# Performance work log

Hardware: AMD Instinct MI355X
Metric: run time of the kernel (lower is better)

The kernel has to match this reference:

```python
import jax, jax.numpy as jnp
import numpy as np

NUM_HEADS = 12
HEAD_DIM = 64
LOGIT_SCALE_MAX = 4.605170185988092  # log(1/0.01), open_clip default
EPS = 1e-12  # F.normalize eps


def setup_inputs() -> dict:
    key = jax.random.key(0)
    ks = jax.random.split(key, 8)
    N, L, C = 2, 2048, 768
    return {
        "x": jax.random.normal(ks[0], (N, L, C), dtype=jnp.float32),
        "in_proj_w": jax.random.normal(ks[1], (3 * C, C), dtype=jnp.float32) * 0.02,
        "in_proj_b": jax.random.normal(ks[2], (3 * C,), dtype=jnp.float32) * 0.02,
        "logit_scale": jax.random.normal(ks[3], (NUM_HEADS, 1, 1), dtype=jnp.float32),
        "learned_scale": jnp.ones((NUM_HEADS,), dtype=jnp.float32),
        "out_proj_w": jax.random.normal(ks[4], (C, C), dtype=jnp.float32) * 0.02,
        "out_proj_b": jax.random.normal(ks[5], (C,), dtype=jnp.float32) * 0.02,
        "attn_mask": jnp.zeros((L, L), dtype=jnp.float32),
    }


def _l2norm(t):
    # F.normalize(dim=-1): x / max(||x||, eps)
    n = jnp.linalg.norm(t, axis=-1, keepdims=True)
    return t / jnp.maximum(n, EPS)


def reference(x, in_proj_w, in_proj_b, logit_scale, learned_scale,
              out_proj_w, out_proj_b, attn_mask):
    N, L, C = x.shape
    H, D = NUM_HEADS, HEAD_DIM
    # packed QKV projection: [N, L, 3C]
    qkv = jnp.einsum("nlc,fc->nlf", x, in_proj_w) + in_proj_b
    q, k, v = jnp.split(qkv, 3, axis=-1)
    # [N, L, C] -> [N, H, L, D]
    to_heads = lambda t: t.reshape(N, L, H, D).transpose(0, 2, 1, 3)
    q, k, v = to_heads(q), to_heads(k), to_heads(v)
    # cosine attention with clamped exp logit scale per head
    attn = jnp.einsum("nhld,nhmd->nhlm", _l2norm(q), _l2norm(k))
    ls = jnp.exp(jnp.minimum(logit_scale, LOGIT_SCALE_MAX))  # [H,1,1]
    attn = attn * ls[None]  # broadcast over [N,H,L,L]
    attn = attn + attn_mask  # additive mask [L,L]
    attn = jax.nn.softmax(attn, axis=-1)
    out = jnp.einsum("nhlm,nhmd->nhld", attn, v)
    # learned per-head output scale
    out = out * learned_scale[None, :, None, None]
    # [N,H,L,D] -> [N,L,C]
    out = out.transpose(0, 2, 1, 3).reshape(N, L, C)
    out = jnp.einsum("nlc,fc->nlf", out, out_proj_w) + out_proj_b
    return out
```

## Files before the change

### kernel.cpp

```cpp
#include <hip/hip_runtime.h>
#include <math.h>

#define NB   2
#define SEQ  2048
#define CH   768
#define NH   12
#define HD   64
#define F3   2304
#define LSMAX 4.605170185988092f
#define LOG2E 1.4426950408889634f

typedef _Float16 f16;
typedef __attribute__((ext_vector_type(8))) _Float16 f16x8;
typedef __attribute__((ext_vector_type(4))) _Float16 f16x4;
typedef __attribute__((ext_vector_type(2))) _Float16 f16x2;
typedef __attribute__((ext_vector_type(4))) float f32x4;
typedef __attribute__((ext_vector_type(16))) float f32x16;

typedef __attribute__((address_space(3))) void lds_void;
typedef __attribute__((address_space(1))) const void gbl_cvoid;

#define QSZ   3145728
#define OATT  (3 * QSZ)
#define XHOFF 12582912
#define W1OFF 15728640
#define W2OFF 17498112
#define FLAGO 18087936

#define VCH   2048
#define VPLN  131072

#define GP2  72

__global__ __launch_bounds__(256) void cvt_f16(const float* __restrict__ X,
                                               const float* __restrict__ W1,
                                               const float* __restrict__ W2,
                                               const float* __restrict__ M,
                                               f16* __restrict__ Xh,
                                               f16* __restrict__ W1h,
                                               f16* __restrict__ W2h,
                                               int* __restrict__ flag)
{
    int tid = blockIdx.x * 256 + threadIdx.x;
    if (blockIdx.y == 3) {
        if (tid < 1048576) {
            float4 v = ((const float4*)M)[tid];
            bool nz = (v.x != 0.f) || (v.y != 0.f) || (v.z != 0.f) || (v.w != 0.f);
            if (__any(nz) && (threadIdx.x & 63) == 0) atomicOr(flag, 1);
        }
        return;
    }
    const float* src; f16* dst; int n4;
    switch (blockIdx.y) {
        case 0:  src = X;  dst = Xh;  n4 = 786432;  break;
        case 1:  src = W1; dst = W1h; n4 = 442368;  break;
        default: src = W2; dst = W2h; n4 = 147456;  break;
    }
    if (tid < n4) {
        float4 v = ((const float4*)src)[tid];
        f16x4 o = {(f16)v.x, (f16)v.y, (f16)v.z, (f16)v.w};
        ((f16x4*)dst)[tid] = o;
    }
}

__global__ __launch_bounds__(256, 4) void qkv_gemm(const f16* __restrict__ Xh,
                                                   const f16* __restrict__ Wh,
                                                   const float* __restrict__ bias,
                                                   const float* __restrict__ logit_scale,
                                                   f16* __restrict__ qkv16)
{
    __shared__ f16 As[2][128 * 32];
    __shared__ f16 Bs[2][128 * 32];
    const int t    = threadIdx.x;
    const int w    = t >> 6;
    const int lane = t & 63;
    const int quad = lane >> 4;
    const int sub  = lane & 15;
    const int wm   = w & 1, wn = w >> 1;
    const int f0   = blockIdx.x * 128;
    const int m0   = blockIdx.y * 128;

    const int s0 = t, s1 = 256 + t;
    const int r0 = s0 >> 2, cb0 = ((s0 & 3) ^ (r0 & 3)) * 8;
    const int r1 = s1 >> 2, cb1 = ((s1 & 3) ^ (r1 & 3)) * 8;
    const f16* ga0 = Xh + (size_t)(m0 + r0) * CH + cb0;
    const f16* ga1 = Xh + (size_t)(m0 + r1) * CH + cb1;
    const f16* gb0 = Wh + (size_t)(f0 + r0) * CH + cb0;
    const f16* gb1 = Wh + (size_t)(f0 + r1) * CH + cb1;

    f32x4 acc[4][4];
#pragma unroll
    for (int i = 0; i < 4; ++i)
#pragma unroll
        for (int j = 0; j < 4; ++j) acc[i][j] = (f32x4){0.f, 0.f, 0.f, 0.f};

    const int pch = (quad ^ (sub & 3)) * 8;

    __builtin_amdgcn_global_load_lds((gbl_cvoid*)(ga0), (lds_void*)&As[0][s0 * 8], 16, 0, 0);
    __builtin_amdgcn_global_load_lds((gbl_cvoid*)(ga1), (lds_void*)&As[0][s1 * 8], 16, 0, 0);
    __builtin_amdgcn_global_load_lds((gbl_cvoid*)(gb0), (lds_void*)&Bs[0][s0 * 8], 16, 0, 0);
    __builtin_amdgcn_global_load_lds((gbl_cvoid*)(gb1), (lds_void*)&Bs[0][s1 * 8], 16, 0, 0);
    __syncthreads();

    for (int k0 = 0; k0 < CH; k0 += 32) {
        const int cur = (k0 >> 5) & 1, nxt = cur ^ 1;
        if (k0 + 32 < CH) {
            __builtin_amdgcn_global_load_lds((gbl_cvoid*)(ga0 + k0 + 32), (lds_void*)&As[nxt][s0 * 8], 16, 0, 0);
            __builtin_amdgcn_global_load_lds((gbl_cvoid*)(ga1 + k0 + 32), (lds_void*)&As[nxt][s1 * 8], 16, 0, 0);
            __builtin_amdgcn_global_load_lds((gbl_cvoid*)(gb0 + k0 + 32), (lds_void*)&Bs[nxt][s0 * 8], 16, 0, 0);
            __builtin_amdgcn_global_load_lds((gbl_cvoid*)(gb1 + k0 + 32), (lds_void*)&Bs[nxt][s1 * 8], 16, 0, 0);
        }
        f16x8 af[4], bf[4];
#pragma unroll
        for (int i = 0; i < 4; ++i) {
            af[i] = *(const f16x8*)&As[cur][(wm * 64 + i * 16 + sub) * 32 + pch];
            bf[i] = *(const f16x8*)&Bs[cur][(wn * 64 + i * 16 + sub) * 32 + pch];
        }
#pragma unroll
        for (int i = 0; i < 4; ++i)
#pragma unroll
            for (int j = 0; j < 4; ++j)
                acc[i][j] = __builtin_amdgcn_mfma_f32_16x16x32_f16(af[i], bf[j], acc[i][j], 0, 0, 0);
        __syncthreads();
    }

    const int t3 = f0 / CH;
    const int h  = ((f0 + wn * 64) % CH) >> 6;
    float bb[4];
#pragma unroll
    for (int j = 0; j < 4; ++j) bb[j] = bias[f0 + wn * 64 + j * 16 + sub];

    if (t3 == 2) {
        f16* vdst = qkv16 + (size_t)2 * QSZ;
#pragma unroll
        for (int i = 0; i < 4; ++i) {
            int mb = m0 + wm * 64 + i * 16 + quad * 4;
            int nn = mb >> 11, l0 = mb & 2047;
            f16* pl = vdst + (size_t)(nn * NH + h) * VPLN + (l0 >> 5) * VCH + (l0 & 31);
#pragma unroll
            for (int j = 0; j < 4; ++j) {
                f16x4 vv;
#pragma unroll
                for (int r = 0; r < 4; ++r) vv[r] = (f16)(acc[i][j][r] + bb[j]);
                *(f16x4*)(pl + (j * 16 + sub) * 32) = vv;
            }
        }
        return;
    }

    f16* dst = qkv16 + (size_t)t3 * QSZ;
    float lsv = (t3 == 0) ? __expf(fminf(logit_scale[h], LSMAX)) * LOG2E : 1.0f;
#pragma unroll
    for (int i = 0; i < 4; ++i) {
#pragma unroll
        for (int r = 0; r < 4; ++r) {
            int m = m0 + wm * 64 + i * 16 + quad * 4 + r;
            int n = m >> 11, l = m & 2047;
            float v[4];
#pragma unroll
            for (int j = 0; j < 4; ++j) v[j] = acc[i][j][r] + bb[j];
            float ss = v[0] * v[0] + v[1] * v[1] + v[2] * v[2] + v[3] * v[3];
#pragma unroll
            for (int mk = 1; mk < 16; mk <<= 1) ss += __shfl_xor(ss, mk, 64);
            float scale = 1.0f / fmaxf(sqrtf(ss), 1e-12f);
            if (t3 == 0) scale *= lsv;
            f16* drow = dst + (((size_t)n * NH + h) * SEQ + l) * HD;
#pragma unroll
            for (int j = 0; j < 4; ++j)
                drow[j * 16 + sub] = (f16)(v[j] * scale);
        }
    }
}

union V8 { f16x4 h[2]; f16x8 v; };
union U8 { int i[4]; f16x8 v; };

__device__ __forceinline__ void compute_chunk(
    const f16x8& k0f, const f16x8& k1f, const f16x8& k2f, const f16x8& k3f,
    const V8& u0v, const V8& u1v, const V8& u2v, const V8& u3v,
    const f16x8& qf0, const f16x8& qf1, const f16x8& qf2, const f16x8& qf3,
    int cc, bool has_mask, const float* __restrict__ Mg, int h2,
    f32x16& o0, f32x16& o1, float& m_run, float& l_acc)
{
    const f16x2 one2 = {(f16)1.f, (f16)1.f};
    f32x16 sA = {};
    sA = __builtin_amdgcn_mfma_f32_32x32x16_f16(k0f, qf0, sA, 0, 0, 0);
    sA = __builtin_amdgcn_mfma_f32_32x32x16_f16(k1f, qf1, sA, 0, 0, 0);
    sA = __builtin_amdgcn_mfma_f32_32x32x16_f16(k2f, qf2, sA, 0, 0, 0);
    sA = __builtin_amdgcn_mfma_f32_32x32x16_f16(k3f, qf3, sA, 0, 0, 0);
    if (has_mask) {
#pragma unroll
        for (int rr = 0; rr < 16; ++rr) {
            int kk = cc * 32 + (rr & 3) + 8 * (rr >> 2) + 4 * h2;
            sA[rr] += LOG2E * Mg[kk];
        }
    }
    float mloc = sA[0];
#pragma unroll
    for (int rr = 1; rr < 16; ++rr) mloc = fmaxf(mloc, sA[rr]);
    float mfull = fmaxf(mloc, __shfl_xor(mloc, 32, 64));
    float mnew = fmaxf(m_run, mfull);
    float al = exp2f(m_run - mnew);
    m_run = mnew;
    l_acc *= al;
#pragma unroll
    for (int rr = 0; rr < 16; ++rr) { o0[rr] *= al; o1[rr] *= al; }
#pragma unroll
    for (int rr = 0; rr < 16; ++rr) sA[rr] = exp2f(sA[rr] - m_run);
#define PK(a, b) ({ f16x2 _t = {(f16)(a), (f16)(b)}; __builtin_bit_cast(int, _t); })
    U8 u0, u1;
    u0.i[0] = PK(sA[0], sA[1]);   u0.i[1] = PK(sA[2], sA[3]);
    u0.i[2] = PK(sA[4], sA[5]);   u0.i[3] = PK(sA[6], sA[7]);
    u1.i[0] = PK(sA[8], sA[9]);   u1.i[1] = PK(sA[10], sA[11]);
    u1.i[2] = PK(sA[12], sA[13]); u1.i[3] = PK(sA[14], sA[15]);
#undef PK
    l_acc = __builtin_amdgcn_fdot2(__builtin_bit_cast(f16x2, u0.i[0]), one2, l_acc, false);
    l_acc = __builtin_amdgcn_fdot2(__builtin_bit_cast(f16x2, u0.i[1]), one2, l_acc, false);
    l_acc = __builtin_amdgcn_fdot2(__builtin_bit_cast(f16x2, u0.i[2]), one2, l_acc, false);
    l_acc = __builtin_amdgcn_fdot2(__builtin_bit_cast(f16x2, u0.i[3]), one2, l_acc, false);
    l_acc = __builtin_amdgcn_fdot2(__builtin_bit_cast(f16x2, u1.i[0]), one2, l_acc, false);
    l_acc = __builtin_amdgcn_fdot2(__builtin_bit_cast(f16x2, u1.i[1]), one2, l_acc, false);
    l_acc = __builtin_amdgcn_fdot2(__builtin_bit_cast(f16x2, u1.i[2]), one2, l_acc, false);
    l_acc = __builtin_amdgcn_fdot2(__builtin_bit_cast(f16x2, u1.i[3]), one2, l_acc, false);
    o0 = __builtin_amdgcn_mfma_f32_32x32x16_f16(u0v.v, u0.v, o0, 0, 0, 0);
    o0 = __builtin_amdgcn_mfma_f32_32x32x16_f16(u1v.v, u1.v, o0, 0, 0, 0);
    o1 = __builtin_amdgcn_mfma_f32_32x32x16_f16(u2v.v, u0.v, o1, 0, 0, 0);
    o1 = __builtin_amdgcn_mfma_f32_32x32x16_f16(u3v.v, u1.v, o1, 0, 0, 0);
}

__global__ __launch_bounds__(256, 3) void attn(const f16* __restrict__ Qh,
                                               const f16* __restrict__ Kh,
                                               const f16* __restrict__ Vt,
                                               const float* __restrict__ M32,
                                               const float* __restrict__ lscale,
                                               const int* __restrict__ flag,
                                               f16* __restrict__ Og)
{
    __shared__ float OS[2][32][68];
    __shared__ float MS[2][32];
    __shared__ float LS[2][32];

    const int t    = threadIdx.x;
    const int w    = t >> 6;
    const int lane = t & 63;
    const int g    = w >> 1;
    const int s    = w & 1;
    const int r32  = lane & 31;
    const int h2   = lane >> 5;
    const int qb   = blockIdx.x * 64;
    const int hh   = blockIdx.y, n = blockIdx.z;
    const bool has_mask = (*flag) != 0;

    const int q = qb + g * 32 + r32;
    const f16* Qg = Qh + ((size_t)(n * NH + hh) * SEQ + q) * HD + 8 * h2;
    const f16* Kl = Kh + ((size_t)(n * NH + hh) * SEQ + s * 1024 + r32) * HD + 8 * h2;
    const f16* Vl = Vt + (size_t)(n * NH + hh) * VPLN + (size_t)(s * 32) * VCH
                       + r32 * 32 + 4 * h2;
    const float* Mg = M32 + (size_t)q * SEQ + s * 1024;

    f16x8 qf0 = *(const f16x8*)(Qg + 0);
    f16x8 qf1 = *(const f16x8*)(Qg + 16);
    f16x8 qf2 = *(const f16x8*)(Qg + 32);
    f16x8 qf3 = *(const f16x8*)(Qg + 48);

#define PREF_K(R0, R1, R2, R3, cc) do {                                   \
    const f16* kp_ = Kl + (size_t)((cc) * 32) * HD;                       \
    R0 = *(const f16x8*)(kp_ + 0);  R1 = *(const f16x8*)(kp_ + 16);       \
    R2 = *(const f16x8*)(kp_ + 32); R3 = *(const f16x8*)(kp_ + 48); } while (0)
#define PREF_V(U0, U1, U2, U3, cc) do {                                   \
    const f16* vp_ = Vl + (cc) * VCH;                                     \
    U0.h[0] = *(const f16x4*)(vp_ + 0);    U0.h[1] = *(const f16x4*)(vp_ + 8);    \
    U1.h[0] = *(const f16x4*)(vp_ + 16);   U1.h[1] = *(const f16x4*)(vp_ + 24);   \
    U2.h[0] = *(const f16x4*)(vp_ + 1024); U2.h[1] = *(const f16x4*)(vp_ + 1032); \
    U3.h[0] = *(const f16x4*)(vp_ + 1040); U3.h[1] = *(const f16x4*)(vp_ + 1048); } while (0)

    f16x8 ka0, ka1, ka2, ka3, kb0, kb1, kb2, kb3;
    V8 ua0, ua1, ua2, ua3, ub0, ub1, ub2, ub3;

    f32x16 o0 = {}, o1 = {};
    float m_run = -1e30f, l_acc = 0.f;

    PREF_K(ka0, ka1, ka2, ka3, 0);
    PREF_V(ua0, ua1, ua2, ua3, 0);
#pragma unroll 1
    for (int c = 0; c < 32; c += 2) {
        PREF_K(kb0, kb1, kb2, kb3, c + 1);
        PREF_V(ub0, ub1, ub2, ub3, c + 1);
        compute_chunk(ka0, ka1, ka2, ka3, ua0, ua1, ua2, ua3,
                      qf0, qf1, qf2, qf3, c, has_mask, Mg, h2,
                      o0, o1, m_run, l_acc);
        if (c + 2 < 32) {
            PREF_K(ka0, ka1, ka2, ka3, c + 2);
            PREF_V(ua0, ua1, ua2, ua3, c + 2);
        }
        compute_chunk(kb0, kb1, kb2, kb3, ub0, ub1, ub2, ub3,
                      qf0, qf1, qf2, qf3, c + 1, has_mask, Mg, h2,
                      o0, o1, m_run, l_acc);
    }
#undef PREF_K
#undef PREF_V

    float l_full = l_acc + __shfl_xor(l_acc, 32, 64);

    if (s == 1) {
        if (h2 == 0) { MS[g][r32] = m_run; LS[g][r32] = l_full; }
#pragma unroll
        for (int rq = 0; rq < 4; ++rq) {
            int d0 = 8 * rq + 4 * h2;
            *(f32x4*)&OS[g][r32][d0] =
                (f32x4){o0[rq * 4 + 0], o0[rq * 4 + 1], o0[rq * 4 + 2], o0[rq * 4 + 3]};
            *(f32x4*)&OS[g][r32][d0 + 32] =
                (f32x4){o1[rq * 4 + 0], o1[rq * 4 + 1], o1[rq * 4 + 2], o1[rq * 4 + 3]};
        }
    }
    __syncthreads();
    if (s == 0) {
        float m_p = MS[g][r32], l_p = LS[g][r32];
        float mm = fmaxf(m_run, m_p);
        float a0 = exp2f(m_run - mm), a1 = exp2f(m_p - mm);
        float l_tot = a0 * l_full + a1 * l_p;
        float sc = lscale[hh] / l_tot;
        float sa = a0 * sc, sb = a1 * sc;
        f16* op = Og + ((size_t)n * SEQ + q) * CH + hh * 64;
#pragma unroll
        for (int rq = 0; rq < 4; ++rq) {
            int d0 = 8 * rq + 4 * h2;
            f32x4 p0 = *(const f32x4*)&OS[g][r32][d0];
            f32x4 p1 = *(const f32x4*)&OS[g][r32][d0 + 32];
            f16x4 ov0, ov1;
#pragma unroll
            for (int j = 0; j < 4; ++j) {
                ov0[j] = (f16)(o0[rq * 4 + j] * sa + p0[j] * sb);
                ov1[j] = (f16)(o1[rq * 4 + j] * sa + p1[j] * sb);
            }
            *(f16x4*)(op + d0)      = ov0;
            *(f16x4*)(op + 32 + d0) = ov1;
        }
    }
}

__global__ __launch_bounds__(256, 4) void out_gemm(const f16* __restrict__ A,
                                                   const f16* __restrict__ Wh,
                                                   const float* __restrict__ bias,
                                                   float* __restrict__ out)
{
    __shared__ f16 As[64 * GP2];
    __shared__ f16 Bs[64 * GP2];
    const int t    = threadIdx.x;
    const int w    = t >> 6;
    const int lane = t & 63;
    const int quad = lane >> 4;
    const int sub  = lane & 15;
    const int f0   = blockIdx.x * 64;
    const int m0   = blockIdx.y * 64;
    const int srow = t >> 2;
    const int sk   = (t & 3) * 16;

    const f16* ag = A + (size_t)(m0 + srow) * CH + sk;
    const f16* bg = Wh + (size_t)(f0 + srow) * CH + sk;
    f16x8 a0 = *(const f16x8*)(ag);
    f16x8 a1 = *(const f16x8*)(ag + 8);
    f16x8 b0 = *(const f16x8*)(bg);
    f16x8 b1 = *(const f16x8*)(bg + 8);

    f32x4 acc[4];
#pragma unroll
    for (int i = 0; i < 4; ++i) acc[i] = (f32x4){0.f, 0.f, 0.f, 0.f};

    for (int k0 = 0; k0 < CH; k0 += 64) {
        __syncthreads();
        *(f16x8*)&As[srow * GP2 + sk + 0] = a0;
        *(f16x8*)&As[srow * GP2 + sk + 8] = a1;
        *(f16x8*)&Bs[srow * GP2 + sk + 0] = b0;
        *(f16x8*)&Bs[srow * GP2 + sk + 8] = b1;
        __syncthreads();
        if (k0 + 64 < CH) {
            a0 = *(const f16x8*)(ag + k0 + 64);
            a1 = *(const f16x8*)(ag + k0 + 72);
            b0 = *(const f16x8*)(bg + k0 + 64);
            b1 = *(const f16x8*)(bg + k0 + 72);
        }
#pragma unroll
        for (int kk = 0; kk < 64; kk += 32) {
            f16x8 bf = *(const f16x8*)&Bs[(w * 16 + sub) * GP2 + kk + quad * 8];
#pragma unroll
            for (int i = 0; i < 4; ++i) {
                f16x8 af = *(const f16x8*)&As[(i * 16 + sub) * GP2 + kk + quad * 8];
                acc[i] = __builtin_amdgcn_mfma_f32_16x16x32_f16(af, bf, acc[i], 0, 0, 0);
            }
        }
    }
    float bb = bias[f0 + w * 16 + sub];
#pragma unroll
    for (int i = 0; i < 4; ++i)
#pragma unroll
        for (int r = 0; r < 4; ++r) {
            int m = m0 + i * 16 + quad * 4 + r;
            out[(size_t)m * CH + f0 + w * 16 + sub] = acc[i][r] + bb;
        }
}

extern "C" void kernel_launch(void* const* d_in, const int* in_sizes, int n_in,
                              void* d_out, int out_size, void* d_ws, size_t ws_size,
                              hipStream_t stream) {
    const float* x    = (const float*)d_in[0];
    const float* w1   = (const float*)d_in[1];
    const float* b1   = (const float*)d_in[2];
    const float* ls   = (const float*)d_in[3];
    const float* lrn  = (const float*)d_in[4];
    const float* w2   = (const float*)d_in[5];
    const float* b2   = (const float*)d_in[6];
    const float* msk  = (const float*)d_in[7];
    f16*   ws16 = (f16*)d_ws;
    int*   flag = (int*)(ws16 + FLAGO);
    float* out  = (float*)d_out;

    (void)hipMemsetAsync(flag, 0, 4, stream);
    hipLaunchKernelGGL(cvt_f16, dim3(4096, 4), dim3(256), 0, stream,
                       x, w1, w2, msk,
                       ws16 + XHOFF, ws16 + W1OFF, ws16 + W2OFF, flag);
    hipLaunchKernelGGL(qkv_gemm, dim3(F3 / 128, (NB * SEQ) / 128), dim3(256), 0, stream,
                       ws16 + XHOFF, ws16 + W1OFF, b1, ls, ws16);
    hipLaunchKernelGGL(attn, dim3(SEQ / 64, NH, NB), dim3(256), 0, stream,
                       ws16, ws16 + QSZ, ws16 + 2 * QSZ, msk, lrn, flag,
                       ws16 + OATT);
    hipLaunchKernelGGL(out_gemm, dim3(CH / 64, (NB * SEQ) / 64), dim3(256), 0, stream,
                       ws16 + OATT, ws16 + W2OFF, b2, out);
}
```

Baseline: 230.0 us.

## Skip softmax rescale under threshold, use raw exp2 and pkrtz, add sched barriers

```diff
diff --git a/kernel.cpp b/kernel.cpp
--- a/kernel.cpp
+++ b/kernel.cpp
@@ -9,6 +9,8 @@
 #define F3   2304
 #define LSMAX 4.605170185988092f
 #define LOG2E 1.4426950408889634f
+#define RESCALE_THR 8.0f
+#define EXP2F(x) __builtin_amdgcn_exp2f(x)
 
 typedef _Float16 f16;
 typedef __attribute__((ext_vector_type(8))) _Float16 f16x8;
@@ -195,25 +197,34 @@
             sA[rr] += LOG2E * Mg[kk];
         }
     }
-    float mloc = sA[0];
-#pragma unroll
-    for (int rr = 1; rr < 16; ++rr) mloc = fmaxf(mloc, sA[rr]);
+    float m = fmaxf(fmaxf(sA[0], sA[1]), sA[2]);
+    m = fmaxf(fmaxf(m, sA[3]), sA[4]);
+    m = fmaxf(fmaxf(m, sA[5]), sA[6]);
+    m = fmaxf(fmaxf(m, sA[7]), sA[8]);
+    m = fmaxf(fmaxf(m, sA[9]), sA[10]);
+    m = fmaxf(fmaxf(m, sA[11]), sA[12]);
+    m = fmaxf(fmaxf(m, sA[13]), sA[14]);
+    float mloc = fmaxf(m, sA[15]);
     float mfull = fmaxf(mloc, __shfl_xor(mloc, 32, 64));
-    float mnew = fmaxf(m_run, mfull);
-    float al = exp2f(m_run - mnew);
-    m_run = mnew;
-    l_acc *= al;
-#pragma unroll
-    for (int rr = 0; rr < 16; ++rr) { o0[rr] *= al; o1[rr] *= al; }
-#pragma unroll
-    for (int rr = 0; rr < 16; ++rr) sA[rr] = exp2f(sA[rr] - m_run);
-#define PK(a, b) ({ f16x2 _t = {(f16)(a), (f16)(b)}; __builtin_bit_cast(int, _t); })
+    if (__any(mfull - m_run > RESCALE_THR)) {
+        float mnew = fmaxf(m_run, mfull);
+        float al = EXP2F(m_run - mnew);
+        m_run = mnew;
+        l_acc *= al;
+#pragma unroll
+        for (int rr = 0; rr < 16; ++rr) { o0[rr] *= al; o1[rr] *= al; }
+    }
+#pragma unroll
+    for (int rr = 0; rr < 16; ++rr) sA[rr] = EXP2F(sA[rr] - m_run);
     U8 u0, u1;
-    u0.i[0] = PK(sA[0], sA[1]);   u0.i[1] = PK(sA[2], sA[3]);
-    u0.i[2] = PK(sA[4], sA[5]);   u0.i[3] = PK(sA[6], sA[7]);
-    u1.i[0] = PK(sA[8], sA[9]);   u1.i[1] = PK(sA[10], sA[11]);
-    u1.i[2] = PK(sA[12], sA[13]); u1.i[3] = PK(sA[14], sA[15]);
-#undef PK
+    u0.i[0] = __builtin_bit_cast(int, __builtin_amdgcn_cvt_pkrtz(sA[0], sA[1]));
+    u0.i[1] = __builtin_bit_cast(int, __builtin_amdgcn_cvt_pkrtz(sA[2], sA[3]));
+    u0.i[2] = __builtin_bit_cast(int, __builtin_amdgcn_cvt_pkrtz(sA[4], sA[5]));
+    u0.i[3] = __builtin_bit_cast(int, __builtin_amdgcn_cvt_pkrtz(sA[6], sA[7]));
+    u1.i[0] = __builtin_bit_cast(int, __builtin_amdgcn_cvt_pkrtz(sA[8], sA[9]));
+    u1.i[1] = __builtin_bit_cast(int, __builtin_amdgcn_cvt_pkrtz(sA[10], sA[11]));
+    u1.i[2] = __builtin_bit_cast(int, __builtin_amdgcn_cvt_pkrtz(sA[12], sA[13]));
+    u1.i[3] = __builtin_bit_cast(int, __builtin_amdgcn_cvt_pkrtz(sA[14], sA[15]));
     l_acc = __builtin_amdgcn_fdot2(__builtin_bit_cast(f16x2, u0.i[0]), one2, l_acc, false);
     l_acc = __builtin_amdgcn_fdot2(__builtin_bit_cast(f16x2, u0.i[1]), one2, l_acc, false);
     l_acc = __builtin_amdgcn_fdot2(__builtin_bit_cast(f16x2, u0.i[2]), one2, l_acc, false);
@@ -282,16 +293,19 @@
 
     PREF_K(ka0, ka1, ka2, ka3, 0);
     PREF_V(ua0, ua1, ua2, ua3, 0);
+    __builtin_amdgcn_sched_barrier(0);
 #pragma unroll 1
     for (int c = 0; c < 32; c += 2) {
         PREF_K(kb0, kb1, kb2, kb3, c + 1);
         PREF_V(ub0, ub1, ub2, ub3, c + 1);
+        __builtin_amdgcn_sched_barrier(0);
         compute_chunk(ka0, ka1, ka2, ka3, ua0, ua1, ua2, ua3,
                       qf0, qf1, qf2, qf3, c, has_mask, Mg, h2,
                       o0, o1, m_run, l_acc);
         if (c + 2 < 32) {
             PREF_K(ka0, ka1, ka2, ka3, c + 2);
             PREF_V(ua0, ua1, ua2, ua3, c + 2);
+            __builtin_amdgcn_sched_barrier(0);
         }
         compute_chunk(kb0, kb1, kb2, kb3, ub0, ub1, ub2, ub3,
                       qf0, qf1, qf2, qf3, c + 1, has_mask, Mg, h2,
@@ -317,7 +331,7 @@
     if (s == 0) {
         float m_p = MS[g][r32], l_p = LS[g][r32];
         float mm = fmaxf(m_run, m_p);
-        float a0 = exp2f(m_run - mm), a1 = exp2f(m_p - mm);
+        float a0 = EXP2F(m_run - mm), a1 = EXP2F(m_p - mm);
         float l_tot = a0 * l_full + a1 * l_p;
         float sc = lscale[hh] / l_tot;
         float sa = a0 * sc, sb = a1 * sc;
```

After: 228.6 us. No clear change (-0.6%).
